# Performance work log

Hardware: AMD Instinct MI355X
Metric: run time of the kernel (lower is better)

## Reference

```python
import jax, jax.numpy as jnp
import numpy as np

# Structure constants C[i, j, k] for the Cl(3,0) geometric product with basis
# order [1, e1, e2, e3, e12, e13, e23, e123]: (a*b)_k = sum_ij a_i b_j C[i,j,k].
_TABLE = [
    (0,0,0,1),(1,1,0,1),(2,2,0,1),(3,3,0,1),(4,4,0,-1),(5,5,0,-1),(6,6,0,-1),(7,7,0,-1),
    (0,1,1,1),(1,0,1,1),(2,4,1,-1),(4,2,1,1),(3,5,1,-1),(5,3,1,1),(6,7,1,-1),(7,6,1,-1),
    (0,2,2,1),(2,0,2,1),(1,4,2,1),(4,1,2,-1),(3,6,2,-1),(6,3,2,1),(5,7,2,1),(7,5,2,1),
    (0,3,3,1),(3,0,3,1),(1,5,3,1),(5,1,3,-1),(2,6,3,1),(6,2,3,-1),(4,7,3,-1),(7,4,3,-1),
    (0,4,4,1),(4,0,4,1),(1,2,4,1),(2,1,4,-1),(3,7,4,1),(7,3,4,1),(5,6,4,-1),(6,5,4,1),
    (0,5,5,1),(5,0,5,1),(1,3,5,1),(3,1,5,-1),(2,7,5,-1),(7,2,5,-1),(4,6,5,1),(6,4,5,-1),
    (0,6,6,1),(6,0,6,1),(2,3,6,1),(3,2,6,-1),(1,7,6,1),(7,1,6,1),(4,5,6,-1),(5,4,6,1),
    (0,7,7,1),(7,0,7,1),(1,6,7,1),(6,1,7,1),(2,5,7,-1),(5,2,7,-1),(3,4,7,1),(4,3,7,1),
]
_C = np.zeros((8, 8, 8), dtype=np.float32)
for _i, _j, _k, _s in _TABLE:
    _C[_i, _j, _k] = _s

B, IN_F, OUT_F = 65536, 64, 64


def setup_inputs() -> dict:
    key = jax.random.key(0)
    ks = jax.random.split(key, 5)
    return {
        "x": jax.random.normal(ks[0], (B, IN_F, 8), dtype=jnp.float32),
        "weight": jax.random.normal(ks[1], (OUT_F, IN_F, 8), dtype=jnp.float32) * 0.02,
        "bias": jnp.zeros((OUT_F, 8), dtype=jnp.float32),
        "row_scale": jax.random.uniform(ks[2], (OUT_F,), dtype=jnp.float32),
        "col_scale": jax.random.uniform(ks[3], (IN_F,), dtype=jnp.float32),
        "bias_shift": jax.random.normal(ks[4], (OUT_F,), dtype=jnp.float32),
    }


def reference(x, weight, bias, row_scale, col_scale, bias_shift):
    C = jnp.asarray(_C)  # [8,8,8] structure constants
    w = weight * row_scale[:, None, None] * col_scale[None, :, None]
    w = jnp.nan_to_num(w, nan=0.0)
    # Fold structure constants into the (small) weight first: wc[o,n,i,k]
    wc = jnp.einsum('onj,ijk->onik', w, C)
    # out[b,o,k] = sum_{n,i} x[b,n,i] * wc[o,n,i,k]  (geometric product + sum over in)
    out = jnp.einsum('bni,onik->bok', x, wc)
    out = out + bias[None]
    out = out.at[..., 0].add(bias_shift[None, :])
    return out
```

## Files before the change

### kernel.cpp

```cpp
#include <hip/hip_runtime.h>
#include <cstdint>

#define M_DIM 65536
#define N_DIM 512
#define K_DIM 512
#define BM 128
#define BN 128
#define BK 32
#define KSTEPS 16
#define NRING 2
#define A_TILE_B (BM * BK * 4)
#define B_TILE_B (4 * BN * 16)
#define LDS_B_OFF (NRING * A_TILE_B)

typedef float f32x4 __attribute__((ext_vector_type(4)));
typedef __bf16 bf16x8 __attribute__((ext_vector_type(8)));
typedef unsigned short us8 __attribute__((ext_vector_type(8)));

__device__ __forceinline__ unsigned short f2bf(float f) {
  unsigned int u = __builtin_bit_cast(unsigned int, f);
  u += 0x7fffu + ((u >> 16) & 1u);
  return (unsigned short)(u >> 16);
}

__device__ __forceinline__ unsigned int cvt_pk_bf16(float lo, float hi) {
  unsigned int r;
  asm("v_cvt_pk_bf16_f32 %0, %1, %2" : "=v"(r) : "v"(lo), "v"(hi));
  return r;
}

__device__ __forceinline__ void async16(const void* g, void* l) {
  __builtin_amdgcn_global_load_lds(
      (const __attribute__((address_space(1))) void*)g,
      (__attribute__((address_space(3))) void*)l, 16, 0, 0);
}

__global__ void clifford_prep(const float* __restrict__ weight,
                              const float* __restrict__ bias,
                              const float* __restrict__ row_scale,
                              const float* __restrict__ col_scale,
                              const float* __restrict__ bias_shift,
                              unsigned short* __restrict__ WCT2,
                              float* __restrict__ bias2) {
  const int t = blockIdx.x * 256 + threadIdx.x;
  if (t < 512) {
    const int o = t >> 3, k = t & 7;
    bias2[t] = bias[t] + (k == 0 ? bias_shift[o] : 0.0f);
  }
  if (t >= 64 * 64) return;
  const int o = t >> 6, n = t & 63;
  const float rs = row_scale[o], cs = col_scale[n];
  float w[8];
#pragma unroll
  for (int j = 0; j < 8; ++j) {
    float v = weight[(size_t)t * 8 + j] * rs * cs;
    w[j] = (v != v) ? 0.0f : v;
  }
  constexpr int TI[64] = {0,1,2,3,4,5,6,7, 0,1,2,4,3,5,6,7, 0,2,1,4,3,6,5,7,
                          0,3,1,5,2,6,4,7, 0,4,1,2,3,7,5,6, 0,5,1,3,2,7,4,6,
                          0,6,2,3,1,7,4,5, 0,7,1,6,2,5,3,4};
  constexpr int TJ[64] = {0,1,2,3,4,5,6,7, 1,0,4,2,5,3,7,6, 2,0,4,1,6,3,7,5,
                          3,0,5,1,6,2,7,4, 4,0,2,1,7,3,6,5, 5,0,3,1,7,2,6,4,
                          6,0,3,2,7,1,5,4, 7,0,6,1,5,2,4,3};
  constexpr int TK[64] = {0,0,0,0,0,0,0,0, 1,1,1,1,1,1,1,1, 2,2,2,2,2,2,2,2,
                          3,3,3,3,3,3,3,3, 4,4,4,4,4,4,4,4, 5,5,5,5,5,5,5,5,
                          6,6,6,6,6,6,6,6, 7,7,7,7,7,7,7,7};
  constexpr float TS[64] = {1,1,1,1,-1,-1,-1,-1, 1,1,-1,1,-1,1,-1,-1, 1,1,1,-1,-1,1,1,1,
                            1,1,1,-1,1,-1,-1,-1, 1,1,1,-1,1,1,-1,1,  1,1,1,-1,-1,-1,1,-1,
                            1,1,1,-1,1,1,-1,1,   1,1,1,1,-1,-1,1,1};
  float wc[8][8];
#pragma unroll
  for (int i = 0; i < 8; ++i)
#pragma unroll
    for (int k = 0; k < 8; ++k) wc[i][k] = 0.0f;
#pragma unroll
  for (int e = 0; e < 64; ++e) wc[TI[e]][TK[e]] += TS[e] * w[TJ[e]];
#pragma unroll
  for (int kb = 0; kb < 8; ++kb)
#pragma unroll
    for (int i = 0; i < 8; ++i)
      WCT2[((size_t)n * N_DIM + o * 8 + kb) * 8 + i] = f2bf(wc[i][kb]);
}

__global__ __launch_bounds__(256, 3) void clifford_gemm(
    const float* __restrict__ x, const unsigned short* __restrict__ WCT2,
    const float* __restrict__ bias2, float* __restrict__ out) {
  __shared__ __align__(16) char lds[NRING * A_TILE_B + NRING * B_TILE_B];

  const int tid = threadIdx.x;
  const int lane = tid & 63;
  const int wv = tid >> 6;

  const int bid = blockIdx.x;
  const int grp = bid >> 5, r = bid & 31;
  const size_t m0 = (size_t)(grp * 8 + (r & 7)) * BM;
  const int n0 = (r >> 3) * BN;

  const int wm = (wv & 1) * 64;
  const int wn = (wv >> 1) * 64;
  const int lm = lane & 15;
  const int kg = lane >> 4;

  const int asw = ((lane & 7) ^ (lane >> 3)) << 4;
  const char* aSrc[4];
#pragma unroll
  for (int c = 0; c < 4; ++c)
    aSrc[c] = (const char*)x +
              (m0 + wv * 32 + c * 8 + (lane >> 3)) * (size_t)(K_DIM * 4) + asw;

  const char* bSrc[2];
#pragma unroll
  for (int c = 0; c < 2; ++c) {
    const int q = c * 2 + (wv >> 1);
    const int nl = (wv & 1) * 64 + lane;
    bSrc[c] = (const char*)WCT2 + ((size_t)q * N_DIM + n0 + nl) * 16;
  }

  const int aRd0 = (wm + lm) * 128 + ((kg * 32 + 0) ^ ((lm & 7) << 4));
  const int aRd1 = (wm + lm) * 128 + ((kg * 32 + 16) ^ ((lm & 7) << 4));
  const int bRd = kg * 2048 + (wn + lm) * 16;

  const f32x4 zero = {0.f, 0.f, 0.f, 0.f};
  f32x4 acc[4][4];
#pragma unroll
  for (int i = 0; i < 4; ++i)
#pragma unroll
    for (int j = 0; j < 4; ++j) acc[i][j] = zero;

  auto issueTile = [&](int ks) {
    const int slot = ks % NRING;
    char* da = &lds[slot * A_TILE_B + wv * 4096];
#pragma unroll
    for (int c = 0; c < 4; ++c)
      async16(aSrc[c] + ks * (BK * 4), da + c * 1024);
    char* db = &lds[LDS_B_OFF + slot * B_TILE_B + wv * 1024];
#pragma unroll
    for (int c = 0; c < 2; ++c)
      async16(bSrc[c] + (size_t)ks * (4 * N_DIM * 16), db + c * 4096);
  };

  issueTile(0);
  issueTile(1);

#pragma unroll
  for (int ks = 0; ks < KSTEPS; ++ks) {
    const int slot = ks % NRING;
    if (ks < KSTEPS - 1)
      asm volatile("s_waitcnt vmcnt(6)" ::: "memory");
    else
      asm volatile("s_waitcnt vmcnt(0)" ::: "memory");
    __builtin_amdgcn_s_barrier();

    f32x4 alo[4], ahi[4];
    us8 bfr[4];
#pragma unroll
    for (int mi = 0; mi < 4; ++mi) {
      alo[mi] = *(const f32x4*)&lds[slot * A_TILE_B + aRd0 + mi * 2048];
      ahi[mi] = *(const f32x4*)&lds[slot * A_TILE_B + aRd1 + mi * 2048];
    }
#pragma unroll
    for (int ni = 0; ni < 4; ++ni)
      bfr[ni] = *(const us8*)&lds[LDS_B_OFF + slot * B_TILE_B + bRd + ni * 256];

    bf16x8 af[4];
#pragma unroll
    for (int mi = 0; mi < 4; ++mi) {
      union { us8 v; unsigned int w[4]; } u;
      u.w[0] = cvt_pk_bf16(alo[mi][0], alo[mi][1]);
      u.w[1] = cvt_pk_bf16(alo[mi][2], alo[mi][3]);
      u.w[2] = cvt_pk_bf16(ahi[mi][0], ahi[mi][1]);
      u.w[3] = cvt_pk_bf16(ahi[mi][2], ahi[mi][3]);
      af[mi] = __builtin_bit_cast(bf16x8, u.v);
    }

    __builtin_amdgcn_s_setprio(1);
#pragma unroll
    for (int mi = 0; mi < 4; ++mi)
#pragma unroll
      for (int ni = 0; ni < 4; ++ni)
        acc[mi][ni] = __builtin_amdgcn_mfma_f32_16x16x32_bf16(
            af[mi], __builtin_bit_cast(bf16x8, bfr[ni]), acc[mi][ni], 0, 0, 0);
    __builtin_amdgcn_s_setprio(0);

    __builtin_amdgcn_sched_barrier(0);
    __builtin_amdgcn_s_barrier();
    if (ks + NRING < KSTEPS) issueTile(ks + NRING);
  }

#pragma unroll
  for (int ni = 0; ni < 4; ++ni) {
    const int nn = n0 + wn + ni * 16 + lm;
    const float b2 = bias2[nn];
#pragma unroll
    for (int mi = 0; mi < 4; ++mi) {
#pragma unroll
      for (int rr = 0; rr < 4; ++rr) {
        const size_t mm = m0 + wm + mi * 16 + kg * 4 + rr;
        out[mm * N_DIM + nn] = acc[mi][ni][rr] + b2;
      }
    }
  }
}

extern "C" void kernel_launch(void* const* d_in, const int* in_sizes, int n_in,
                              void* d_out, int out_size, void* d_ws, size_t ws_size,
                              hipStream_t stream) {
  const float* x          = (const float*)d_in[0];
  const float* weight     = (const float*)d_in[1];
  const float* bias       = (const float*)d_in[2];
  const float* row_scale  = (const float*)d_in[3];
  const float* col_scale  = (const float*)d_in[4];
  const float* bias_shift = (const float*)d_in[5];

  unsigned short* WCT2 = (unsigned short*)d_ws;
  float* bias2 = (float*)((char*)d_ws + (size_t)N_DIM * K_DIM * 2);

  clifford_prep<<<16, 256, 0, stream>>>(weight, bias, row_scale, col_scale,
                                        bias_shift, WCT2, bias2);
  clifford_gemm<<<(M_DIM / BM) * (N_DIM / BN), 256, 0, stream>>>(
      x, WCT2, bias2, (float*)d_out);
}
```

Before: 262.6 us.

## Make GEMM persistent over four M tiles with cross-tile prefetch and vector stores

The GEMM launches 512 blocks, and each block loops over four M tiles spaced 1024 rows apart. The first K tiles of the next M tile are prefetched during the last K steps of the current one, so the pipeline does not drain between tiles. The MFMA operands are swapped, which transposes the accumulator layout and lets the epilogue write contiguous float4 stores with the bias preloaded as vectors. Blocks are mapped with an XCD-aware index, and occupancy is lowered to 2 blocks per SIMD via launch bounds. The risks are fewer resident waves and fewer blocks than before, which could leave CUs unevenly loaded.

New measurement: 285.5 us. 8.7% more time.

```diff
diff --git a/kernel.cpp b/kernel.cpp
--- a/kernel.cpp
+++ b/kernel.cpp
@@ -7,11 +7,11 @@
 #define BM 128
 #define BN 128
 #define BK 32
-#define KSTEPS 16
 #define NRING 2
 #define A_TILE_B (BM * BK * 4)
 #define B_TILE_B (4 * BN * 16)
 #define LDS_B_OFF (NRING * A_TILE_B)
+#define TILE_ADV (8 * BM * K_DIM * 4)
 
 typedef float f32x4 __attribute__((ext_vector_type(4)));
 typedef __bf16 bf16x8 __attribute__((ext_vector_type(8)));
@@ -82,7 +82,7 @@
       WCT2[((size_t)n * N_DIM + o * 8 + kb) * 8 + i] = f2bf(wc[i][kb]);
 }
 
-__global__ __launch_bounds__(256, 3) void clifford_gemm(
+__global__ __launch_bounds__(256, 2) void clifford_gemm(
     const float* __restrict__ x, const unsigned short* __restrict__ WCT2,
     const float* __restrict__ bias2, float* __restrict__ out) {
   __shared__ __align__(16) char lds[NRING * A_TILE_B + NRING * B_TILE_B];
@@ -92,9 +92,12 @@
   const int wv = tid >> 6;
 
   const int bid = blockIdx.x;
-  const int grp = bid >> 5, r = bid & 31;
-  const size_t m0 = (size_t)(grp * 8 + (r & 7)) * BM;
-  const int n0 = (r >> 3) * BN;
+  const int xcd = bid & 7;
+  const int jj = bid >> 3;
+  const int nt = jj & 3;
+  const int mc = jj >> 2;
+  const int n0 = nt * BN;
+  const size_t m0r = (size_t)(mc * 32 + xcd) * BM;
 
   const int wm = (wv & 1) * 64;
   const int wn = (wv >> 1) * 64;
@@ -102,11 +105,11 @@
   const int kg = lane >> 4;
 
   const int asw = ((lane & 7) ^ (lane >> 3)) << 4;
-  const char* aSrc[4];
+  const char* aT[4];
 #pragma unroll
   for (int c = 0; c < 4; ++c)
-    aSrc[c] = (const char*)x +
-              (m0 + wv * 32 + c * 8 + (lane >> 3)) * (size_t)(K_DIM * 4) + asw;
+    aT[c] = (const char*)x +
+            (m0r + wv * 32 + c * 8 + (lane >> 3)) * (size_t)(K_DIM * 4) + asw;
 
   const char* bSrc[2];
 #pragma unroll
@@ -120,6 +123,11 @@
   const int aRd1 = (wm + lm) * 128 + ((kg * 32 + 16) ^ ((lm & 7) << 4));
   const int bRd = kg * 2048 + (wn + lm) * 16;
 
+  f32x4 bv[4];
+#pragma unroll
+  for (int ni = 0; ni < 4; ++ni)
+    bv[ni] = *(const f32x4*)(bias2 + n0 + wn + ni * 16 + kg * 4);
+
   const f32x4 zero = {0.f, 0.f, 0.f, 0.f};
   f32x4 acc[4][4];
 #pragma unroll
@@ -127,78 +135,91 @@
 #pragma unroll
     for (int j = 0; j < 4; ++j) acc[i][j] = zero;
 
-  auto issueTile = [&](int ks) {
-    const int slot = ks % NRING;
+  auto issueTile = [&](const char* const ap[4], int ksIdx) {
+    const int slot = ksIdx & 1;
     char* da = &lds[slot * A_TILE_B + wv * 4096];
 #pragma unroll
     for (int c = 0; c < 4; ++c)
-      async16(aSrc[c] + ks * (BK * 4), da + c * 1024);
+      async16(ap[c] + ksIdx * (BK * 4), da + c * 1024);
     char* db = &lds[LDS_B_OFF + slot * B_TILE_B + wv * 1024];
 #pragma unroll
     for (int c = 0; c < 2; ++c)
-      async16(bSrc[c] + (size_t)ks * (4 * N_DIM * 16), db + c * 4096);
+      async16(bSrc[c] + (size_t)ksIdx * (4 * N_DIM * 16), db + c * 4096);
   };
 
-  issueTile(0);
-  issueTile(1);
-
-#pragma unroll
-  for (int ks = 0; ks < KSTEPS; ++ks) {
-    const int slot = ks % NRING;
-    if (ks < KSTEPS - 1)
-      asm volatile("s_waitcnt vmcnt(6)" ::: "memory");
-    else
-      asm volatile("s_waitcnt vmcnt(0)" ::: "memory");
-    __builtin_amdgcn_s_barrier();
-
-    f32x4 alo[4], ahi[4];
-    us8 bfr[4];
-#pragma unroll
-    for (int mi = 0; mi < 4; ++mi) {
-      alo[mi] = *(const f32x4*)&lds[slot * A_TILE_B + aRd0 + mi * 2048];
-      ahi[mi] = *(const f32x4*)&lds[slot * A_TILE_B + aRd1 + mi * 2048];
-    }
-#pragma unroll
-    for (int ni = 0; ni < 4; ++ni)
-      bfr[ni] = *(const us8*)&lds[LDS_B_OFF + slot * B_TILE_B + bRd + ni * 256];
-
-    bf16x8 af[4];
-#pragma unroll
-    for (int mi = 0; mi < 4; ++mi) {
-      union { us8 v; unsigned int w[4]; } u;
-      u.w[0] = cvt_pk_bf16(alo[mi][0], alo[mi][1]);
-      u.w[1] = cvt_pk_bf16(alo[mi][2], alo[mi][3]);
-      u.w[2] = cvt_pk_bf16(ahi[mi][0], ahi[mi][1]);
-      u.w[3] = cvt_pk_bf16(ahi[mi][2], ahi[mi][3]);
-      af[mi] = __builtin_bit_cast(bf16x8, u.v);
-    }
-
-    __builtin_amdgcn_s_setprio(1);
-#pragma unroll
-    for (int mi = 0; mi < 4; ++mi)
+  issueTile(aT, 0);
+  issueTile(aT, 1);
+
+  for (int t = 0; t < 4; ++t) {
+    const char* aT2[4];
+#pragma unroll
+    for (int c = 0; c < 4; ++c) aT2[c] = aT[c] + TILE_ADV;
+
+#pragma unroll
+    for (int ks = 0; ks < 16; ++ks) {
+      const int slot = ks & 1;
+      if (t == 3 && ks == 15)
+        asm volatile("s_waitcnt vmcnt(0)" ::: "memory");
+      else if (ks <= 1 && t > 0)
+        asm volatile("s_waitcnt vmcnt(22)" ::: "memory");
+      else
+        asm volatile("s_waitcnt vmcnt(6)" ::: "memory");
+      __builtin_amdgcn_s_barrier();
+
+      f32x4 alo[4], ahi[4];
+      us8 bfr[4];
+#pragma unroll
+      for (int mi = 0; mi < 4; ++mi) {
+        alo[mi] = *(const f32x4*)&lds[slot * A_TILE_B + aRd0 + mi * 2048];
+        ahi[mi] = *(const f32x4*)&lds[slot * A_TILE_B + aRd1 + mi * 2048];
+      }
 #pragma unroll
       for (int ni = 0; ni < 4; ++ni)
-        acc[mi][ni] = __builtin_amdgcn_mfma_f32_16x16x32_bf16(
-            af[mi], __builtin_bit_cast(bf16x8, bfr[ni]), acc[mi][ni], 0, 0, 0);
-    __builtin_amdgcn_s_setprio(0);
-
-    __builtin_amdgcn_sched_barrier(0);
-    __builtin_amdgcn_s_barrier();
-    if (ks + NRING < KSTEPS) issueTile(ks + NRING);
-  }
-
-#pragma unroll
-  for (int ni = 0; ni < 4; ++ni) {
-    const int nn = n0 + wn + ni * 16 + lm;
-    const float b2 = bias2[nn];
-#pragma unroll
-    for (int mi = 0; mi < 4; ++mi) {
-#pragma unroll
-      for (int rr = 0; rr < 4; ++rr) {
-        const size_t mm = m0 + wm + mi * 16 + kg * 4 + rr;
-        out[mm * N_DIM + nn] = acc[mi][ni][rr] + b2;
+        bfr[ni] = *(const us8*)&lds[LDS_B_OFF + slot * B_TILE_B + bRd + ni * 256];
+
+      bf16x8 af[4];
+#pragma unroll
+      for (int mi = 0; mi < 4; ++mi) {
+        union { us8 v; unsigned int w[4]; } u;
+        u.w[0] = cvt_pk_bf16(alo[mi][0], alo[mi][1]);
+        u.w[1] = cvt_pk_bf16(alo[mi][2], alo[mi][3]);
+        u.w[2] = cvt_pk_bf16(ahi[mi][0], ahi[mi][1]);
+        u.w[3] = cvt_pk_bf16(ahi[mi][2], ahi[mi][3]);
+        af[mi] = __builtin_bit_cast(bf16x8, u.v);
+      }
+
+      __builtin_amdgcn_s_setprio(1);
+#pragma unroll
+      for (int mi = 0; mi < 4; ++mi)
+#pragma unroll
+        for (int ni = 0; ni < 4; ++ni)
+          acc[mi][ni] = __builtin_amdgcn_mfma_f32_16x16x32_bf16(
+              __builtin_bit_cast(bf16x8, bfr[ni]), af[mi], acc[mi][ni], 0, 0, 0);
+      __builtin_amdgcn_s_setprio(0);
+
+      __builtin_amdgcn_sched_barrier(0);
+      __builtin_amdgcn_s_barrier();
+
+      if (ks < 14)
+        issueTile(aT, ks + 2);
+      else if (t < 3)
+        issueTile(aT2, ks - 14);
+
+      if (ks == 15) {
+        float* ob = out + (m0r + (size_t)t * 1024 + wm + lm) * N_DIM +
+                    n0 + wn + kg * 4;
+#pragma unroll
+        for (int mi = 0; mi < 4; ++mi)
+#pragma unroll
+          for (int ni = 0; ni < 4; ++ni) {
+            f32x4 v = acc[mi][ni] + bv[ni];
+            *(f32x4*)(ob + mi * 16 * N_DIM + ni * 16) = v;
+            acc[mi][ni] = zero;
+          }
       }
     }
+#pragma unroll
+    for (int c = 0; c < 4; ++c) aT[c] = aT2[c];
   }
 }
 
@@ -217,6 +238,5 @@
 
   clifford_prep<<<16, 256, 0, stream>>>(weight, bias, row_scale, col_scale,
                                         bias_shift, WCT2, bias2);
-  clifford_gemm<<<(M_DIM / BM) * (N_DIM / BN), 256, 0, stream>>>(
-      x, WCT2, bias2, (float*)d_out);
-}
+  clifford_gemm<<<512, 256, 0, stream>>>(x, WCT2, bias2, (float*)d_out);
+}
```
